# Kernel tuning notes

Hardware: AMD Instinct MI355X
Metric: run time of the kernel (lower is better)

The kernel has to match this reference:

```python
import jax, jax.numpy as jnp
import numpy as np
from jax import lax

B, A, H, W = 16, 9, 128, 128
STRIDE = 16
MIN_SIZE = 16.0


def _generate_anchors():
    base = 16.0
    ratios = np.array([0.5, 1.0, 2.0])
    scales = np.array([8.0, 16.0, 32.0])
    ctr = (base - 1.0) / 2.0
    size = base * base
    ws0 = np.round(np.sqrt(size / ratios))
    hs0 = np.round(ws0 * ratios)
    ws = (ws0[:, None] * scales[None, :]).reshape(-1)  # [9]
    hs = (hs0[:, None] * scales[None, :]).reshape(-1)
    base_anchors = np.stack([ctr - 0.5 * (ws - 1), ctr - 0.5 * (hs - 1),
                             ctr + 0.5 * (ws - 1), ctr + 0.5 * (hs - 1)], axis=1)  # [9,4]
    sx = np.arange(W) * STRIDE
    sy = np.arange(H) * STRIDE
    shift_x, shift_y = np.meshgrid(sx, sy)  # [H,W]
    shifts = np.stack([shift_x, shift_y, shift_x, shift_y], axis=-1).reshape(H * W, 1, 4)
    return (shifts + base_anchors[None]).reshape(-1, 4).astype(np.float32)  # [H*W*A,4]


def setup_inputs() -> dict:
    key = jax.random.key(0)
    k1, k2 = jax.random.split(key)
    scores = jax.random.normal(k1, (B, 2 * A, H, W), jnp.float32)
    bbox_deltas = jax.random.normal(k2, (B, 4 * A, H, W), jnp.float32) * 0.1
    anchors = jnp.asarray(_generate_anchors())
    im_info = jnp.tile(jnp.array([H * STRIDE, W * STRIDE, 1.0, 1.0], jnp.float32), (B, 1))
    return {"scores": scores, "bbox_deltas": bbox_deltas, "anchors": anchors,
            "im_info": im_info, "num_anchors": A, "pre_nms": 2000, "post_nms": 300,
            "nms_thresh": 0.7}


def _iou_matrix(b):
    x1, y1, x2, y2 = b[:, 0], b[:, 1], b[:, 2], b[:, 3]
    area = (x2 - x1 + 1.0) * (y2 - y1 + 1.0)
    iw = jnp.maximum(jnp.minimum(x2[:, None], x2[None, :]) - jnp.maximum(x1[:, None], x1[None, :]) + 1.0, 0.0)
    ih = jnp.maximum(jnp.minimum(y2[:, None], y2[None, :]) - jnp.maximum(y1[:, None], y1[None, :]) + 1.0, 0.0)
    inter = iw * ih
    return inter / (area[:, None] + area[None, :] - inter)


def reference(scores, bbox_deltas, anchors, im_info, num_anchors, pre_nms, post_nms, nms_thresh):
    batch = bbox_deltas.shape[0]
    feat_w = scores.shape[3]
    # deltas -> [B, H*W*A, 4]
    deltas = bbox_deltas.transpose(0, 2, 3, 1).reshape(batch, -1, 4)
    # fg/bg softmax exactly as in the module
    s = jax.nn.softmax(scores.reshape(batch, 2, -1, feat_w), axis=1)
    s = s.reshape(batch, num_anchors * 2, -1, feat_w)[:, num_anchors:, :, :]
    s = s.transpose(0, 2, 3, 1).reshape(batch, -1)  # [B, H*W*A]
    anc = jnp.broadcast_to(anchors.reshape(1, -1, 4), deltas.shape)
    # bbox_transform_inv
    widths = anc[..., 2] - anc[..., 0] + 1.0
    heights = anc[..., 3] - anc[..., 1] + 1.0
    ctr_x = anc[..., 0] + 0.5 * widths
    ctr_y = anc[..., 1] + 0.5 * heights
    dx, dy, dw, dh = deltas[..., 0], deltas[..., 1], deltas[..., 2], deltas[..., 3]
    pcx = dx * widths + ctr_x
    pcy = dy * heights + ctr_y
    pw = jnp.exp(dw) * widths
    ph = jnp.exp(dh) * heights
    proposals = jnp.stack([pcx - 0.5 * pw, pcy - 0.5 * ph, pcx + 0.5 * pw, pcy + 0.5 * ph], axis=-1)
    # clip_boxes to image extent (im_info = [h, w, sy, sx])
    w_max = (im_info[:, 1] - 1.0)[:, None]
    h_max = (im_info[:, 0] - 1.0)[:, None]
    proposals = jnp.stack([
        jnp.clip(proposals[..., 0], 0.0, w_max),
        jnp.clip(proposals[..., 1], 0.0, h_max),
        jnp.clip(proposals[..., 2], 0.0, w_max),
        jnp.clip(proposals[..., 3], 0.0, h_max)], axis=-1)

    ar = jnp.arange(pre_nms)

    def per_image(props, scr, info):
        ws = props[:, 2] - props[:, 0] + 1.0
        hs = props[:, 3] - props[:, 1] + 1.0
        valid = (ws >= MIN_SIZE * info[3]) & (hs >= MIN_SIZE * info[2])
        masked = jnp.where(valid, scr, -jnp.inf)
        vals, idx = lax.top_k(masked, pre_nms)  # sort desc + truncate to pre_nms
        boxes = props[idx]  # [pre_nms, 4], score-sorted
        live = jnp.isfinite(vals)  # drop filtered boxes if fewer than pre_nms survive
        iou = _iou_matrix(boxes)  # [pre_nms, pre_nms]
        def body(i, keep):
            sup = keep[i] & (iou[i] > nms_thresh) & (ar > i)
            return keep & (~sup)
        keep = lax.fori_loop(0, pre_nms, body, live)  # greedy NMS over sorted boxes
        pos = jnp.where(keep, jnp.cumsum(keep) - 1, post_nms)
        kept = jnp.zeros((post_nms, 4), boxes.dtype).at[pos].set(boxes, mode='drop')
        return kept

    kept = jax.vmap(per_image)(proposals, s, im_info)  # [B, post_nms, 4]
    bidx = jnp.broadcast_to(jnp.arange(batch, dtype=kept.dtype)[:, None, None], (batch, post_nms, 1))
    output = jnp.concatenate([bidx, kept], axis=-1)  # [B, post_nms, 5]
    return output, proposals
```

## Files before the change

### kernel.cpp

```cpp
#include <hip/hip_runtime.h>
#include <stdint.h>

#define B_ 16
#define A_ 9
#define H_ 128
#define W_ 128
#define HW_ (H_*W_)
#define N_ (HW_*A_)
#define PRE_ 2000
#define POST_ 300
#define CAND_CAP 4096
#define SEG_ 32

typedef unsigned int u32;
typedef unsigned long long u64;

#define OFF_STATE  0ull
#define OFF_HIST0  1024ull
#define OFF_HIST1  (OFF_HIST0 + 16384ull)
#define OFF_KEYS   (OFF_HIST1 + 16384ull)
#define OFF_CAND   (OFF_KEYS + (u64)B_*N_*4)
#define OFF_SELBOX (OFF_CAND + (u64)B_*CAND_CAP*8)
#define OFF_LIVE   (OFF_SELBOX + (u64)B_*PRE_*16)
#define OFF_SUPP   (OFF_LIVE + (u64)B_*32*8)

__device__ __forceinline__ u32 mono_key(float f) {
    u32 u = __float_as_uint(f);
    return (u & 0x80000000u) ? ~u : (u | 0x80000000u);
}

__device__ __forceinline__ void wave_select256(const u32* __restrict__ hh, u32 need,
                                               u32* __restrict__ out) {
    int lane = threadIdx.x & 63;
    uint4 hv = ((const uint4*)hh)[lane];
    u32 psum = hv.x + hv.y + hv.z + hv.w;
    u32 s = psum;
    #pragma unroll
    for (int off = 1; off < 64; off <<= 1) {
        u32 o = (u32)__shfl_down((int)s, off);
        if (lane + off < 64) s += o;
    }
    u32 S_next = (u32)__shfl_down((int)s, 1);
    if (lane == 63) S_next = 0;
    u32 above[4], cnt[4];
    above[3] = S_next;             cnt[3] = hv.w;
    above[2] = S_next + hv.w;      cnt[2] = hv.z;
    above[1] = above[2] + hv.z;    cnt[1] = hv.y;
    above[0] = above[1] + hv.y;    cnt[0] = hv.x;
    #pragma unroll
    for (int j = 3; j >= 0; --j) {
        if (above[j] < need && above[j] + cnt[j] >= need) {
            out[0] = (u32)(4*lane + j);
            out[1] = need - above[j];
        }
    }
}

__global__ __launch_bounds__(576) void decode_kernel(
        const float* __restrict__ scores,
        const float* __restrict__ deltas,
        const float* __restrict__ anchors,
        const float* __restrict__ im_info,
        float* __restrict__ outprop,
        u32* __restrict__ keys,
        u32* __restrict__ hist0) {
    __shared__ float4 tile[9][65];
    __shared__ float4 sbase[A_];
    __shared__ u32 h[256];
    int tid = threadIdx.x;
    int a = tid >> 6, lane = tid & 63;
    if (tid < A_) sbase[tid] = ((const float4*)anchors)[tid];
    if (tid < 256) h[tid] = 0;
    __syncthreads();

    int b  = blockIdx.x >> 8;
    int pb = blockIdx.x & 255;
    int p0 = pb << 6;
    int p  = p0 + lane;

    float s0 = scores[((b*2*A_ + a)      << 14) + p];
    float s1 = scores[((b*2*A_ + A_ + a) << 14) + p];
    float m  = fmaxf(s0, s1);
    float e0 = expf(s0 - m);
    float e1 = expf(s1 - m);
    float fg = e1 / (e0 + e1);

    float4 base = sbase[a];
    int ix = p & (W_-1), iy = p >> 7;
    float sx = (float)(ix * 16), sy = (float)(iy * 16);
    float ax1 = base.x + sx, ay1 = base.y + sy, ax2 = base.z + sx, ay2 = base.w + sy;

    float w  = ax2 - ax1 + 1.0f;
    float h_ = ay2 - ay1 + 1.0f;
    float cx = ax1 + 0.5f*w;
    float cy = ay1 + 0.5f*h_;

    const float* dbase = deltas + (u64)(((b*4*A_ + 4*a) << 14) + p);
    float dx = dbase[0];
    float dy = dbase[HW_];
    float dw = dbase[2*HW_];
    float dh = dbase[3*HW_];

    float pcx = dx*w  + cx;
    float pcy = dy*h_ + cy;
    float pw  = expf(dw)*w;
    float ph  = expf(dh)*h_;
    float x1 = pcx - 0.5f*pw, y1 = pcy - 0.5f*ph;
    float x2 = pcx + 0.5f*pw, y2 = pcy + 0.5f*ph;

    float wmax = im_info[b*4 + 1] - 1.0f;
    float hmax = im_info[b*4 + 0] - 1.0f;
    x1 = fminf(fmaxf(x1, 0.0f), wmax);
    y1 = fminf(fmaxf(y1, 0.0f), hmax);
    x2 = fminf(fmaxf(x2, 0.0f), wmax);
    y2 = fminf(fmaxf(y2, 0.0f), hmax);

    tile[a][lane] = make_float4(x1, y1, x2, y2);

    float bw = x2 - x1 + 1.0f;
    float bh = y2 - y1 + 1.0f;
    bool valid = (bw >= 16.0f*im_info[b*4 + 3]) && (bh >= 16.0f*im_info[b*4 + 2]);
    float sc = valid ? fg : -__builtin_inff();
    u32 k = mono_key(sc);
    keys[((u64)(b*A_ + a) << 14) + p] = k;
    atomicAdd(&h[k >> 24], 1u);
    __syncthreads();

    int a2 = tid % 9, pl = tid / 9;
    ((float4*)outprop)[(u64)b*N_ + p0*9 + tid] = tile[a2][pl];

    if (tid < 256 && h[tid]) atomicAdd(&hist0[b*256 + tid], h[tid]);
}

__global__ __launch_bounds__(1024) void hist16_kernel(
        const u32* __restrict__ keys, const u32* __restrict__ hist0,
        u32* __restrict__ hist1) {
    int b = blockIdx.x >> 4;
    int slice = blockIdx.x & 15;
    int tid = threadIdx.x;
    __shared__ u32 sel[2];
    __shared__ u32 h[256];
    if (tid < 64) wave_select256(hist0 + b*256, (u32)PRE_, sel);
    for (int i = tid; i < 256; i += 1024) h[i] = 0;
    __syncthreads();
    u32 pfx = sel[0];
    const u32* kb = keys + (u64)b*N_ + slice*(N_/16);
    for (int n = tid; n < N_/16; n += 1024) {
        u32 k = kb[n];
        if ((k >> 24) == pfx) atomicAdd(&h[(k >> 16) & 255u], 1u);
    }
    __syncthreads();
    for (int i = tid; i < 256; i += 1024)
        if (h[i]) atomicAdd(&hist1[b*256 + i], h[i]);
}

__global__ __launch_bounds__(1024) void collect_kernel(
        const u32* __restrict__ keys, const u32* __restrict__ hist0,
        const u32* __restrict__ hist1, u32* __restrict__ state,
        u64* __restrict__ cand) {
    int b = blockIdx.x >> 4;
    int slice = blockIdx.x & 15;
    int tid = threadIdx.x;
    int wave = tid >> 6, lane = tid & 63;
    __shared__ u32 sel8[2], sel16[2];
    __shared__ u32 wbase[16];
    __shared__ u32 s_base;
    if (tid < 64) wave_select256(hist0 + b*256, (u32)PRE_, sel8);
    __syncthreads();
    if (tid < 64) wave_select256(hist1 + b*256, sel8[1], sel16);
    __syncthreads();
    u32 T = (sel8[0] << 24) | (sel16[0] << 16);

    const u32* kb = keys + (u64)b*N_ + slice*(N_/16);
    u64* cb = cand + (u64)b*CAND_CAP;

    u32 kreg[9];
    int c = 0;
    #pragma unroll
    for (int r = 0; r < 9; ++r) {
        kreg[r] = kb[tid + r*1024];
        c += (kreg[r] >= T) ? 1 : 0;
    }

    int x = c;
    #pragma unroll
    for (int off = 1; off < 64; off <<= 1) {
        int y = __shfl_up(x, off);
        if (lane >= off) x += y;
    }
    if (lane == 63) wbase[wave] = (u32)x;
    __syncthreads();
    if (tid == 0) {
        u32 acc = 0;
        #pragma unroll
        for (int w2 = 0; w2 < 16; ++w2) { u32 t2 = wbase[w2]; wbase[w2] = acc; acc += t2; }
        s_base = acc ? atomicAdd(&state[b*8 + 2], acc) : 0u;
    }
    __syncthreads();

    u32 pos = s_base + wbase[wave] + (u32)(x - c);
    #pragma unroll
    for (int r = 0; r < 9; ++r) {
        if (kreg[r] >= T) {
            int idx = slice*(N_/16) + tid + r*1024;
            u32 n = (u32)((idx & (HW_-1))*A_ + (idx >> 14));
            if (pos < CAND_CAP) cb[pos] = ((u64)kreg[r] << 32) | (u32)(~n);
            pos++;
        }
    }
}

__global__ __launch_bounds__(1024) void rank_kernel(
        const u64* __restrict__ cand, const u32* __restrict__ state,
        const float* __restrict__ outprop,
        float4* __restrict__ selbox, u32* __restrict__ selkey) {
    int bi = blockIdx.x;
    int b = bi >> 4, chunk = bi & 15;
    int tid = threadIdx.x;
    int q = tid >> 8, ti = tid & 255;
    __shared__ __align__(16) u64 sc[CAND_CAP];
    __shared__ u32 prank[256];

    u32 cnt = state[b*8 + 2];
    if (cnt > CAND_CAP) cnt = CAND_CAP;
    const u64* cb = cand + (u64)b*CAND_CAP;
    for (int j = tid; j < CAND_CAP; j += 1024) sc[j] = (j < (int)cnt) ? cb[j] : 0ull;
    if (tid < 256) prank[tid] = 0;
    __syncthreads();

    int i = (chunk << 8) + ti;
    u64 mine = sc[i];

    int pairs = ((int)cnt + 1) >> 1;
    int pq = (pairs + 3) >> 2;
    int p0 = q * pq;
    int p1 = p0 + pq; if (p1 > pairs) p1 = pairs;
    const ulonglong2* sl = (const ulonglong2*)sc;
    u32 c = 0;
    #pragma unroll 8
    for (int p = p0; p < p1; ++p) {
        ulonglong2 v = sl[p];
        c += (v.x > mine) ? 1u : 0u;
        c += (v.y > mine) ? 1u : 0u;
    }
    if (c) atomicAdd(&prank[ti], c);
    __syncthreads();

    if (q == 0 && i < (int)cnt) {
        u32 rank = prank[ti];
        if (rank < PRE_) {
            u32 n = ~(u32)mine;
            float4 box = ((const float4*)outprop)[(u64)b*N_ + n];
            selbox[(u64)b*PRE_ + rank] = box;
            selkey[b*2048 + rank] = (u32)(mine >> 32);
        }
    }
}

__global__ __launch_bounds__(256) void iou_kernel(
        const float4* __restrict__ selbox, const float* __restrict__ thrp,
        u64* __restrict__ supp) {
    int bi = blockIdx.x;
    int b = bi / 250;
    int rbase = (bi % 250) * 8;
    int c0 = rbase >> 8;
    int tid = threadIdx.x;
    __shared__ float4 box[PRE_];
    for (int i = (c0 << 8) + tid; i < PRE_; i += 256) box[i] = selbox[(u64)b*PRE_ + i];
    __syncthreads();
    float thresh = thrp[0];
    int wv = tid >> 6, lane = tid & 63;

    float4 p[8]; float ai[8];
    #pragma unroll
    for (int r = 0; r < 8; ++r) {
        p[r]  = box[rbase + r];
        ai[r] = (p[r].z - p[r].x + 1.f) * (p[r].w - p[r].y + 1.f);
    }
    for (int c = c0; c < 8; ++c) {
        int j = c*256 + tid;
        bool inb = (j < PRE_);
        float4 q = box[inb ? j : 0];
        float aj = (q.z - q.x + 1.f) * (q.w - q.y + 1.f);
        #pragma unroll
        for (int r = 0; r < 8; ++r) {
            float iw = fminf(p[r].z, q.z) - fmaxf(p[r].x, q.x) + 1.f;
            float ih = fminf(p[r].w, q.w) - fmaxf(p[r].y, q.y) + 1.f;
            float inter = fmaxf(iw, 0.f) * ih;
            float su = ai[r] + aj;
            float un = su - inter;
            float m  = __fmaf_rn(-thresh, un, inter);
            bool pred = m > 0.0f;
            if (__any(fabsf(m) <= 2.0f)) {
                pred = (inter / un) > thresh;
            }
            pred = pred && inb;
            u64 ball = __ballot(pred);
            if (lane == 0)
                supp[((u64)(b*PRE_ + rbase + r))*32 + (c*4 + wv)] = ball;
        }
    }
}

__global__ __launch_bounds__(256, 1) void scan_kernel(
        const u64* __restrict__ supp, const u32* __restrict__ selkey,
        const float4* __restrict__ selbox, float* __restrict__ out0) {
    int b = blockIdx.x;
    int tid = threadIdx.x;
    int wave = tid >> 6, lane = tid & 63;

    __shared__ u64 rbuf[2][64][33];
    __shared__ u64 lwords[32];
    __shared__ u64 keptmask[SEG_];
    __shared__ int kept[POST_];
    __shared__ int s_kc;

    #pragma unroll
    for (int k = 0; k < 8; ++k) {
        int r = k*256 + tid;
        u32 kk = selkey[b*2048 + r];
        u64 bal = __ballot((r < PRE_) && (kk >= 0x80000000u));
        if (lane == 0) lwords[k*4 + wave] = bal;
    }
    if (tid < SEG_) keptmask[tid] = 0ull;
    if (tid == 0) s_kc = 0;

    const u64* sb = supp + (u64)b*PRE_*32;
    int widx = tid - 64;

    u64 gr[11];
    if (wave != 0) {
        #pragma unroll
        for (int k = 0; k < 11; ++k) {
            int f = k*192 + widx;
            if (f < 2048) gr[k] = sb[(u64)(f >> 5)*32 + (f & 31)];
        }
        #pragma unroll
        for (int k = 0; k < 11; ++k) {
            int f = k*192 + widx;
            if (f < 2048) rbuf[0][f >> 5][f & 31] = gr[k];
        }
        #pragma unroll
        for (int k = 0; k < 11; ++k) {
            int f = k*192 + widx;
            if (f < 2048) gr[k] = sb[(u64)(64 + (f >> 5))*32 + (f & 31)];
        }
    }
    __syncthreads();

    u64 aliveW = 0ull;
    if (wave == 0 && lane < 32) aliveW = lwords[lane];
    int kc = 0;
    int ll = lane & 31;

    for (int g = 0; g < SEG_; ++g) {
        int cur = g & 1;
        if (wave != 0) {
            if (g + 1 < SEG_) {
                #pragma unroll
                for (int k = 0; k < 11; ++k) {
                    int f = k*192 + widx;
                    if (f < 2048) rbuf[cur ^ 1][f >> 5][f & 31] = gr[k];
                }
            }
            if (g + 2 < SEG_) {
                #pragma unroll
                for (int k = 0; k < 11; ++k) {
                    int f = k*192 + widx;
                    if (f < 2048) {
                        int row = ((g + 2) << 6) + (f >> 5);
                        if (row > PRE_ - 1) row = PRE_ - 1;
                        gr[k] = sb[(u64)row*32 + (f & 31)];
                    }
                }
            }
        } else {
            u64 dj = rbuf[cur][lane][g];
            u32 djlo = (u32)dj, djhi = (u32)(dj >> 32);
            u32 alo = __builtin_amdgcn_readlane((u32)aliveW, g);
            u32 ahi = __builtin_amdgcn_readlane((u32)(aliveW >> 32), g);
            u64 a_s = ((u64)ahi << 32) | alo;
            if (a_s) {
                u64 ks = 0ull;
                while (a_s && kc < POST_) {
                    int i = (int)__builtin_ctzll(a_s);
                    u32 kml = __builtin_amdgcn_readlane(djlo, i);
                    u32 kmh = __builtin_amdgcn_readlane(djhi, i);
                    u64 km = ((u64)kmh << 32) | kml;
                    ks |= (1ull << i);
                    kc++;
                    a_s &= ~km;
                    a_s &= ~(1ull << i);
                }
                if (lane == 0) keptmask[g] = ks;
                if (kc < POST_) {
                    u64 t = ks, orr = 0ull;
                    while (t) {
                        int i0 = (int)__builtin_ctzll(t);
                        #define GJ(n) int j##n = t ? (int)__builtin_ctzll(t) : i0; if (t) t &= t - 1;
                        GJ(0) GJ(1) GJ(2) GJ(3) GJ(4) GJ(5) GJ(6) GJ(7)
                        #undef GJ
                        u64 r0 = rbuf[cur][j0][ll];
                        u64 r1 = rbuf[cur][j1][ll];
                        u64 r2 = rbuf[cur][j2][ll];
                        u64 r3 = rbuf[cur][j3][ll];
                        u64 r4 = rbuf[cur][j4][ll];
                        u64 r5 = rbuf[cur][j5][ll];
                        u64 r6 = rbuf[cur][j6][ll];
                        u64 r7 = rbuf[cur][j7][ll];
                        orr |= ((r0 | r1) | (r2 | r3)) | ((r4 | r5) | (r6 | r7));
                    }
                    aliveW &= ~orr;
                }
            }
            if (lane == 0) s_kc = kc;
        }
        __syncthreads();
        bool done = (wave == 0) ? (kc >= POST_) : (s_kc >= POST_);
        if (done) break;
    }

    if (wave == 0) {
        u64 w = (lane < 32) ? keptmask[lane] : 0ull;
        int pc = (int)__builtin_popcountll(w);
        int x = pc;
        #pragma unroll
        for (int off = 1; off < 64; off <<= 1) {
            int y = __shfl_up(x, off);
            if (lane >= off) x += y;
        }
        int pr = x - pc;
        u64 t = w;
        int c = 0;
        while (t) {
            int bit = (int)__builtin_ctzll(t);
            t &= t - 1;
            int pos = pr + c; c++;
            if (pos < POST_) kept[pos] = lane*64 + bit;
        }
    }
    __syncthreads();

    int kc2 = s_kc;
    for (int r = tid; r < POST_; r += 256) {
        int i = (r < kc2) ? kept[r] : -1;
        float o1 = 0.f, o2 = 0.f, o3 = 0.f, o4 = 0.f;
        if (i >= 0) {
            float4 bx = selbox[(u64)b*PRE_ + i];
            o1 = bx.x; o2 = bx.y; o3 = bx.z; o4 = bx.w;
        }
        float* rowp = out0 + (u64)(b*POST_ + r)*5;
        rowp[0] = (float)b;
        rowp[1] = o1; rowp[2] = o2; rowp[3] = o3; rowp[4] = o4;
    }
}

extern "C" void kernel_launch(void* const* d_in, const int* in_sizes, int n_in,
                              void* d_out, int out_size, void* d_ws, size_t ws_size,
                              hipStream_t stream) {
    const float* scores  = (const float*)d_in[0];
    const float* deltas  = (const float*)d_in[1];
    const float* anchors = (const float*)d_in[2];
    const float* im_info = (const float*)d_in[3];
    const float* thrp    = (const float*)d_in[7];

    float* out0    = (float*)d_out;
    float* outprop = out0 + (u64)B_*POST_*5;

    char* ws = (char*)d_ws;
    u32*    state  = (u32*)   (ws + OFF_STATE);
    u32*    hist0  = (u32*)   (ws + OFF_HIST0);
    u32*    hist1  = (u32*)   (ws + OFF_HIST1);
    u32*    keys   = (u32*)   (ws + OFF_KEYS);
    u64*    cand   = (u64*)   (ws + OFF_CAND);
    float4* selbox = (float4*)(ws + OFF_SELBOX);
    u64*    supp   = (u64*)   (ws + OFF_SUPP);
    u32*    selkey = (u32*)   (ws + OFF_KEYS);

    hipMemsetAsync(ws, 0, OFF_KEYS, stream);

    decode_kernel<<<B_*256, 576, 0, stream>>>(scores, deltas, anchors, im_info, outprop, keys, hist0);
    hist16_kernel<<<B_*16, 1024, 0, stream>>>(keys, hist0, hist1);
    collect_kernel<<<B_*16, 1024, 0, stream>>>(keys, hist0, hist1, state, cand);
    rank_kernel<<<B_*16, 1024, 0, stream>>>(cand, state, outprop, selbox, selkey);
    iou_kernel<<<B_*250, 256, 0, stream>>>(selbox, thrp, supp);
    scan_kernel<<<B_, 256, 0, stream>>>(supp, selkey, selbox, out0);
}
```

Baseline: 222.7 us.

## Fuse histogram, collect, rank, IoU and NMS scan into one cooperative kernel

Replaces the five post-decode kernels with a single cooperative kernel launched on 256 blocks of 1024 threads, separating the stages with grid-wide syncs and sharing one shared-memory union across stages. Keys are loaded into registers once and reused for both the second histogram and candidate collection, so the keys array is no longer read twice. The IoU stage is remapped so each block covers several 8-row strips, and the scan stage runs on the first 16 blocks with more loader waves. The aim is to cut per-launch overhead and redundant global reads. In exchange it adds grid-sync cost, requires co-residency of all blocks, and the 1024-thread launch bounds may raise register pressure in the IoU phase.

```diff
diff --git a/kernel.cpp b/kernel.cpp
--- a/kernel.cpp
+++ b/kernel.cpp
@@ -1,5 +1,8 @@
 #include <hip/hip_runtime.h>
+#include <hip/hip_cooperative_groups.h>
 #include <stdint.h>
+
+namespace cg = cooperative_groups;
 
 #define B_ 16
 #define A_ 9
@@ -132,326 +135,306 @@
     if (tid < 256 && h[tid]) atomicAdd(&hist0[b*256 + tid], h[tid]);
 }
 
-__global__ __launch_bounds__(1024) void hist16_kernel(
+__global__ __launch_bounds__(1024, 4) void fused_kernel(
         const u32* __restrict__ keys, const u32* __restrict__ hist0,
-        u32* __restrict__ hist1) {
-    int b = blockIdx.x >> 4;
-    int slice = blockIdx.x & 15;
-    int tid = threadIdx.x;
-    __shared__ u32 sel[2];
-    __shared__ u32 h[256];
-    if (tid < 64) wave_select256(hist0 + b*256, (u32)PRE_, sel);
-    for (int i = tid; i < 256; i += 1024) h[i] = 0;
-    __syncthreads();
-    u32 pfx = sel[0];
-    const u32* kb = keys + (u64)b*N_ + slice*(N_/16);
-    for (int n = tid; n < N_/16; n += 1024) {
-        u32 k = kb[n];
-        if ((k >> 24) == pfx) atomicAdd(&h[(k >> 16) & 255u], 1u);
-    }
-    __syncthreads();
-    for (int i = tid; i < 256; i += 1024)
-        if (h[i]) atomicAdd(&hist1[b*256 + i], h[i]);
-}
-
-__global__ __launch_bounds__(1024) void collect_kernel(
-        const u32* __restrict__ keys, const u32* __restrict__ hist0,
-        const u32* __restrict__ hist1, u32* __restrict__ state,
-        u64* __restrict__ cand) {
-    int b = blockIdx.x >> 4;
-    int slice = blockIdx.x & 15;
+        u32* __restrict__ hist1, u32* __restrict__ state,
+        u64* __restrict__ cand, const float* __restrict__ outprop,
+        float4* __restrict__ selbox, u32* __restrict__ selkey,
+        const float* __restrict__ thrp, u64* __restrict__ supp,
+        float* __restrict__ out0) {
+    cg::grid_group grid = cg::this_grid();
+    int bi = blockIdx.x;
+    int b = bi >> 4, slice = bi & 15;
     int tid = threadIdx.x;
     int wave = tid >> 6, lane = tid & 63;
-    __shared__ u32 sel8[2], sel16[2];
-    __shared__ u32 wbase[16];
-    __shared__ u32 s_base;
-    if (tid < 64) wave_select256(hist0 + b*256, (u32)PRE_, sel8);
+
+    __shared__ union SM {
+        struct { u32 h[256]; } p1;
+        struct { u64 sc[CAND_CAP]; u32 prank[256]; } p3;
+        struct { float4 box[PRE_]; } p4;
+        struct { u64 rbuf[2][64][33]; u64 lwords[32];
+                 u64 keptmask[SEG_]; int kept[POST_]; int s_kc; } p5;
+    } sm;
+    __shared__ u32 xsel8[2], xsel16[2], xwbase[16];
+    __shared__ u32 xsbase;
+
+    if (tid < 64) wave_select256(hist0 + b*256, (u32)PRE_, xsel8);
+    for (int i = tid; i < 256; i += 1024) sm.p1.h[i] = 0;
     __syncthreads();
-    if (tid < 64) wave_select256(hist1 + b*256, sel8[1], sel16);
-    __syncthreads();
-    u32 T = (sel8[0] << 24) | (sel16[0] << 16);
-
+    u32 pfx = xsel8[0];
     const u32* kb = keys + (u64)b*N_ + slice*(N_/16);
-    u64* cb = cand + (u64)b*CAND_CAP;
-
     u32 kreg[9];
-    int c = 0;
     #pragma unroll
     for (int r = 0; r < 9; ++r) {
         kreg[r] = kb[tid + r*1024];
-        c += (kreg[r] >= T) ? 1 : 0;
-    }
-
-    int x = c;
-    #pragma unroll
-    for (int off = 1; off < 64; off <<= 1) {
-        int y = __shfl_up(x, off);
-        if (lane >= off) x += y;
-    }
-    if (lane == 63) wbase[wave] = (u32)x;
+        if ((kreg[r] >> 24) == pfx) atomicAdd(&sm.p1.h[(kreg[r] >> 16) & 255u], 1u);
+    }
     __syncthreads();
-    if (tid == 0) {
-        u32 acc = 0;
+    for (int i = tid; i < 256; i += 1024)
+        if (sm.p1.h[i]) atomicAdd(&hist1[b*256 + i], sm.p1.h[i]);
+
+    grid.sync();
+
+    if (tid < 64) wave_select256(hist1 + b*256, xsel8[1], xsel16);
+    __syncthreads();
+    {
+        u32 T = (xsel8[0] << 24) | (xsel16[0] << 16);
+        int c = 0;
         #pragma unroll
-        for (int w2 = 0; w2 < 16; ++w2) { u32 t2 = wbase[w2]; wbase[w2] = acc; acc += t2; }
-        s_base = acc ? atomicAdd(&state[b*8 + 2], acc) : 0u;
-    }
-    __syncthreads();
-
-    u32 pos = s_base + wbase[wave] + (u32)(x - c);
-    #pragma unroll
-    for (int r = 0; r < 9; ++r) {
-        if (kreg[r] >= T) {
-            int idx = slice*(N_/16) + tid + r*1024;
-            u32 n = (u32)((idx & (HW_-1))*A_ + (idx >> 14));
-            if (pos < CAND_CAP) cb[pos] = ((u64)kreg[r] << 32) | (u32)(~n);
-            pos++;
-        }
-    }
-}
-
-__global__ __launch_bounds__(1024) void rank_kernel(
-        const u64* __restrict__ cand, const u32* __restrict__ state,
-        const float* __restrict__ outprop,
-        float4* __restrict__ selbox, u32* __restrict__ selkey) {
-    int bi = blockIdx.x;
-    int b = bi >> 4, chunk = bi & 15;
-    int tid = threadIdx.x;
-    int q = tid >> 8, ti = tid & 255;
-    __shared__ __align__(16) u64 sc[CAND_CAP];
-    __shared__ u32 prank[256];
-
-    u32 cnt = state[b*8 + 2];
-    if (cnt > CAND_CAP) cnt = CAND_CAP;
-    const u64* cb = cand + (u64)b*CAND_CAP;
-    for (int j = tid; j < CAND_CAP; j += 1024) sc[j] = (j < (int)cnt) ? cb[j] : 0ull;
-    if (tid < 256) prank[tid] = 0;
-    __syncthreads();
-
-    int i = (chunk << 8) + ti;
-    u64 mine = sc[i];
-
-    int pairs = ((int)cnt + 1) >> 1;
-    int pq = (pairs + 3) >> 2;
-    int p0 = q * pq;
-    int p1 = p0 + pq; if (p1 > pairs) p1 = pairs;
-    const ulonglong2* sl = (const ulonglong2*)sc;
-    u32 c = 0;
-    #pragma unroll 8
-    for (int p = p0; p < p1; ++p) {
-        ulonglong2 v = sl[p];
-        c += (v.x > mine) ? 1u : 0u;
-        c += (v.y > mine) ? 1u : 0u;
-    }
-    if (c) atomicAdd(&prank[ti], c);
-    __syncthreads();
-
-    if (q == 0 && i < (int)cnt) {
-        u32 rank = prank[ti];
-        if (rank < PRE_) {
-            u32 n = ~(u32)mine;
-            float4 box = ((const float4*)outprop)[(u64)b*N_ + n];
-            selbox[(u64)b*PRE_ + rank] = box;
-            selkey[b*2048 + rank] = (u32)(mine >> 32);
-        }
-    }
-}
-
-__global__ __launch_bounds__(256) void iou_kernel(
-        const float4* __restrict__ selbox, const float* __restrict__ thrp,
-        u64* __restrict__ supp) {
-    int bi = blockIdx.x;
-    int b = bi / 250;
-    int rbase = (bi % 250) * 8;
-    int c0 = rbase >> 8;
-    int tid = threadIdx.x;
-    __shared__ float4 box[PRE_];
-    for (int i = (c0 << 8) + tid; i < PRE_; i += 256) box[i] = selbox[(u64)b*PRE_ + i];
-    __syncthreads();
-    float thresh = thrp[0];
-    int wv = tid >> 6, lane = tid & 63;
-
-    float4 p[8]; float ai[8];
-    #pragma unroll
-    for (int r = 0; r < 8; ++r) {
-        p[r]  = box[rbase + r];
-        ai[r] = (p[r].z - p[r].x + 1.f) * (p[r].w - p[r].y + 1.f);
-    }
-    for (int c = c0; c < 8; ++c) {
-        int j = c*256 + tid;
-        bool inb = (j < PRE_);
-        float4 q = box[inb ? j : 0];
-        float aj = (q.z - q.x + 1.f) * (q.w - q.y + 1.f);
-        #pragma unroll
-        for (int r = 0; r < 8; ++r) {
-            float iw = fminf(p[r].z, q.z) - fmaxf(p[r].x, q.x) + 1.f;
-            float ih = fminf(p[r].w, q.w) - fmaxf(p[r].y, q.y) + 1.f;
-            float inter = fmaxf(iw, 0.f) * ih;
-            float su = ai[r] + aj;
-            float un = su - inter;
-            float m  = __fmaf_rn(-thresh, un, inter);
-            bool pred = m > 0.0f;
-            if (__any(fabsf(m) <= 2.0f)) {
-                pred = (inter / un) > thresh;
-            }
-            pred = pred && inb;
-            u64 ball = __ballot(pred);
-            if (lane == 0)
-                supp[((u64)(b*PRE_ + rbase + r))*32 + (c*4 + wv)] = ball;
-        }
-    }
-}
-
-__global__ __launch_bounds__(256, 1) void scan_kernel(
-        const u64* __restrict__ supp, const u32* __restrict__ selkey,
-        const float4* __restrict__ selbox, float* __restrict__ out0) {
-    int b = blockIdx.x;
-    int tid = threadIdx.x;
-    int wave = tid >> 6, lane = tid & 63;
-
-    __shared__ u64 rbuf[2][64][33];
-    __shared__ u64 lwords[32];
-    __shared__ u64 keptmask[SEG_];
-    __shared__ int kept[POST_];
-    __shared__ int s_kc;
-
-    #pragma unroll
-    for (int k = 0; k < 8; ++k) {
-        int r = k*256 + tid;
-        u32 kk = selkey[b*2048 + r];
-        u64 bal = __ballot((r < PRE_) && (kk >= 0x80000000u));
-        if (lane == 0) lwords[k*4 + wave] = bal;
-    }
-    if (tid < SEG_) keptmask[tid] = 0ull;
-    if (tid == 0) s_kc = 0;
-
-    const u64* sb = supp + (u64)b*PRE_*32;
-    int widx = tid - 64;
-
-    u64 gr[11];
-    if (wave != 0) {
-        #pragma unroll
-        for (int k = 0; k < 11; ++k) {
-            int f = k*192 + widx;
-            if (f < 2048) gr[k] = sb[(u64)(f >> 5)*32 + (f & 31)];
-        }
-        #pragma unroll
-        for (int k = 0; k < 11; ++k) {
-            int f = k*192 + widx;
-            if (f < 2048) rbuf[0][f >> 5][f & 31] = gr[k];
-        }
-        #pragma unroll
-        for (int k = 0; k < 11; ++k) {
-            int f = k*192 + widx;
-            if (f < 2048) gr[k] = sb[(u64)(64 + (f >> 5))*32 + (f & 31)];
-        }
-    }
-    __syncthreads();
-
-    u64 aliveW = 0ull;
-    if (wave == 0 && lane < 32) aliveW = lwords[lane];
-    int kc = 0;
-    int ll = lane & 31;
-
-    for (int g = 0; g < SEG_; ++g) {
-        int cur = g & 1;
-        if (wave != 0) {
-            if (g + 1 < SEG_) {
-                #pragma unroll
-                for (int k = 0; k < 11; ++k) {
-                    int f = k*192 + widx;
-                    if (f < 2048) rbuf[cur ^ 1][f >> 5][f & 31] = gr[k];
-                }
-            }
-            if (g + 2 < SEG_) {
-                #pragma unroll
-                for (int k = 0; k < 11; ++k) {
-                    int f = k*192 + widx;
-                    if (f < 2048) {
-                        int row = ((g + 2) << 6) + (f >> 5);
-                        if (row > PRE_ - 1) row = PRE_ - 1;
-                        gr[k] = sb[(u64)row*32 + (f & 31)];
-                    }
-                }
-            }
-        } else {
-            u64 dj = rbuf[cur][lane][g];
-            u32 djlo = (u32)dj, djhi = (u32)(dj >> 32);
-            u32 alo = __builtin_amdgcn_readlane((u32)aliveW, g);
-            u32 ahi = __builtin_amdgcn_readlane((u32)(aliveW >> 32), g);
-            u64 a_s = ((u64)ahi << 32) | alo;
-            if (a_s) {
-                u64 ks = 0ull;
-                while (a_s && kc < POST_) {
-                    int i = (int)__builtin_ctzll(a_s);
-                    u32 kml = __builtin_amdgcn_readlane(djlo, i);
-                    u32 kmh = __builtin_amdgcn_readlane(djhi, i);
-                    u64 km = ((u64)kmh << 32) | kml;
-                    ks |= (1ull << i);
-                    kc++;
-                    a_s &= ~km;
-                    a_s &= ~(1ull << i);
-                }
-                if (lane == 0) keptmask[g] = ks;
-                if (kc < POST_) {
-                    u64 t = ks, orr = 0ull;
-                    while (t) {
-                        int i0 = (int)__builtin_ctzll(t);
-                        #define GJ(n) int j##n = t ? (int)__builtin_ctzll(t) : i0; if (t) t &= t - 1;
-                        GJ(0) GJ(1) GJ(2) GJ(3) GJ(4) GJ(5) GJ(6) GJ(7)
-                        #undef GJ
-                        u64 r0 = rbuf[cur][j0][ll];
-                        u64 r1 = rbuf[cur][j1][ll];
-                        u64 r2 = rbuf[cur][j2][ll];
-                        u64 r3 = rbuf[cur][j3][ll];
-                        u64 r4 = rbuf[cur][j4][ll];
-                        u64 r5 = rbuf[cur][j5][ll];
-                        u64 r6 = rbuf[cur][j6][ll];
-                        u64 r7 = rbuf[cur][j7][ll];
-                        orr |= ((r0 | r1) | (r2 | r3)) | ((r4 | r5) | (r6 | r7));
-                    }
-                    aliveW &= ~orr;
-                }
-            }
-            if (lane == 0) s_kc = kc;
-        }
-        __syncthreads();
-        bool done = (wave == 0) ? (kc >= POST_) : (s_kc >= POST_);
-        if (done) break;
-    }
-
-    if (wave == 0) {
-        u64 w = (lane < 32) ? keptmask[lane] : 0ull;
-        int pc = (int)__builtin_popcountll(w);
-        int x = pc;
+        for (int r = 0; r < 9; ++r) c += (kreg[r] >= T) ? 1 : 0;
+        int x = c;
         #pragma unroll
         for (int off = 1; off < 64; off <<= 1) {
             int y = __shfl_up(x, off);
             if (lane >= off) x += y;
         }
-        int pr = x - pc;
-        u64 t = w;
-        int c = 0;
-        while (t) {
-            int bit = (int)__builtin_ctzll(t);
-            t &= t - 1;
-            int pos = pr + c; c++;
-            if (pos < POST_) kept[pos] = lane*64 + bit;
-        }
-    }
-    __syncthreads();
-
-    int kc2 = s_kc;
-    for (int r = tid; r < POST_; r += 256) {
-        int i = (r < kc2) ? kept[r] : -1;
-        float o1 = 0.f, o2 = 0.f, o3 = 0.f, o4 = 0.f;
-        if (i >= 0) {
-            float4 bx = selbox[(u64)b*PRE_ + i];
-            o1 = bx.x; o2 = bx.y; o3 = bx.z; o4 = bx.w;
-        }
-        float* rowp = out0 + (u64)(b*POST_ + r)*5;
-        rowp[0] = (float)b;
-        rowp[1] = o1; rowp[2] = o2; rowp[3] = o3; rowp[4] = o4;
+        if (lane == 63) xwbase[wave] = (u32)x;
+        __syncthreads();
+        if (tid == 0) {
+            u32 acc = 0;
+            #pragma unroll
+            for (int w2 = 0; w2 < 16; ++w2) { u32 t2 = xwbase[w2]; xwbase[w2] = acc; acc += t2; }
+            xsbase = acc ? atomicAdd(&state[b*8 + 2], acc) : 0u;
+        }
+        __syncthreads();
+        u32 pos = xsbase + xwbase[wave] + (u32)(x - c);
+        u64* cb = cand + (u64)b*CAND_CAP;
+        #pragma unroll
+        for (int r = 0; r < 9; ++r) {
+            if (kreg[r] >= T) {
+                int idx = slice*(N_/16) + tid + r*1024;
+                u32 n = (u32)((idx & (HW_-1))*A_ + (idx >> 14));
+                if (pos < CAND_CAP) cb[pos] = ((u64)kreg[r] << 32) | (u32)(~n);
+                pos++;
+            }
+        }
+    }
+
+    grid.sync();
+
+    {
+        int q = tid >> 8, ti = tid & 255;
+        u32 cnt = state[b*8 + 2];
+        if (cnt > CAND_CAP) cnt = CAND_CAP;
+        const u64* cb = cand + (u64)b*CAND_CAP;
+        for (int j = tid; j < CAND_CAP; j += 1024) sm.p3.sc[j] = (j < (int)cnt) ? cb[j] : 0ull;
+        if (tid < 256) sm.p3.prank[tid] = 0;
+        __syncthreads();
+        int i = (slice << 8) + ti;
+        u64 mine = sm.p3.sc[i];
+        int pairs = ((int)cnt + 1) >> 1;
+        int pq = (pairs + 3) >> 2;
+        int p0 = q * pq;
+        int p1 = p0 + pq; if (p1 > pairs) p1 = pairs;
+        const ulonglong2* sl = (const ulonglong2*)sm.p3.sc;
+        u32 c = 0;
+        #pragma unroll 8
+        for (int p = p0; p < p1; ++p) {
+            ulonglong2 v = sl[p];
+            c += (v.x > mine) ? 1u : 0u;
+            c += (v.y > mine) ? 1u : 0u;
+        }
+        if (c) atomicAdd(&sm.p3.prank[ti], c);
+        __syncthreads();
+        if (q == 0 && i < (int)cnt) {
+            u32 rank = sm.p3.prank[ti];
+            if (rank < PRE_) {
+                u32 n = ~(u32)mine;
+                float4 box = ((const float4*)outprop)[(u64)b*N_ + n];
+                selbox[(u64)b*PRE_ + rank] = box;
+                selkey[b*2048 + rank] = (u32)(mine >> 32);
+            }
+        }
+    }
+
+    grid.sync();
+
+    {
+        float thresh = thrp[0];
+        for (int i = tid; i < PRE_; i += 1024) sm.p4.box[i] = selbox[(u64)b*PRE_ + i];
+        __syncthreads();
+        int q = tid >> 8, tq = tid & 255;
+        int wv = (tq >> 6), ln = tq & 63;
+        for (int it = 0; it < 4; ++it) {
+            int strip = slice*4 + q + it*64;
+            if (strip >= 250) break;
+            int rbase = strip * 8;
+            int c0 = rbase >> 8;
+            float4 p[8]; float ai[8];
+            #pragma unroll
+            for (int r = 0; r < 8; ++r) {
+                p[r]  = sm.p4.box[rbase + r];
+                ai[r] = (p[r].z - p[r].x + 1.f) * (p[r].w - p[r].y + 1.f);
+            }
+            for (int c = c0; c < 8; ++c) {
+                int j = c*256 + tq;
+                bool inb = (j < PRE_);
+                float4 qq = sm.p4.box[inb ? j : 0];
+                float aj = (qq.z - qq.x + 1.f) * (qq.w - qq.y + 1.f);
+                #pragma unroll
+                for (int r = 0; r < 8; ++r) {
+                    float iw = fminf(p[r].z, qq.z) - fmaxf(p[r].x, qq.x) + 1.f;
+                    float ih = fminf(p[r].w, qq.w) - fmaxf(p[r].y, qq.y) + 1.f;
+                    float inter = fmaxf(iw, 0.f) * ih;
+                    float su = ai[r] + aj;
+                    float un = su - inter;
+                    float mm = __fmaf_rn(-thresh, un, inter);
+                    bool pred = mm > 0.0f;
+                    if (__any(fabsf(mm) <= 2.0f)) {
+                        pred = (inter / un) > thresh;
+                    }
+                    pred = pred && inb;
+                    u64 ball = __ballot(pred);
+                    if (ln == 0)
+                        supp[((u64)(b*PRE_ + rbase + r))*32 + (c*4 + wv)] = ball;
+                }
+            }
+        }
+    }
+
+    grid.sync();
+
+    if (bi >= B_) return;
+    int b5 = bi;
+    {
+        #pragma unroll
+        for (int k = 0; k < 2; ++k) {
+            int r = k*1024 + tid;
+            u32 kk = selkey[b5*2048 + r];
+            u64 bal = __ballot((r < PRE_) && (kk >= 0x80000000u));
+            if (lane == 0) sm.p5.lwords[k*16 + wave] = bal;
+        }
+        if (tid < SEG_) sm.p5.keptmask[tid] = 0ull;
+        if (tid == 0) sm.p5.s_kc = 0;
+
+        const u64* sb = supp + (u64)b5*PRE_*32;
+        int widx = tid - 64;
+
+        u64 gr[3];
+        if (wave != 0) {
+            #pragma unroll
+            for (int k = 0; k < 3; ++k) {
+                int f = k*960 + widx;
+                if (f < 2048) gr[k] = sb[(u64)(f >> 5)*32 + (f & 31)];
+            }
+            #pragma unroll
+            for (int k = 0; k < 3; ++k) {
+                int f = k*960 + widx;
+                if (f < 2048) sm.p5.rbuf[0][f >> 5][f & 31] = gr[k];
+            }
+            #pragma unroll
+            for (int k = 0; k < 3; ++k) {
+                int f = k*960 + widx;
+                if (f < 2048) gr[k] = sb[(u64)(64 + (f >> 5))*32 + (f & 31)];
+            }
+        }
+        __syncthreads();
+
+        u64 aliveW = 0ull;
+        if (wave == 0 && lane < 32) aliveW = sm.p5.lwords[lane];
+        int kc = 0;
+        int ll = lane & 31;
+
+        for (int g = 0; g < SEG_; ++g) {
+            int cur = g & 1;
+            if (wave != 0) {
+                if (g + 1 < SEG_) {
+                    #pragma unroll
+                    for (int k = 0; k < 3; ++k) {
+                        int f = k*960 + widx;
+                        if (f < 2048) sm.p5.rbuf[cur ^ 1][f >> 5][f & 31] = gr[k];
+                    }
+                }
+                if (g + 2 < SEG_) {
+                    #pragma unroll
+                    for (int k = 0; k < 3; ++k) {
+                        int f = k*960 + widx;
+                        if (f < 2048) {
+                            int row = ((g + 2) << 6) + (f >> 5);
+                            if (row > PRE_ - 1) row = PRE_ - 1;
+                            gr[k] = sb[(u64)row*32 + (f & 31)];
+                        }
+                    }
+                }
+            } else {
+                u64 dj = sm.p5.rbuf[cur][lane][g];
+                u32 djlo = (u32)dj, djhi = (u32)(dj >> 32);
+                u32 alo = __builtin_amdgcn_readlane((u32)aliveW, g);
+                u32 ahi = __builtin_amdgcn_readlane((u32)(aliveW >> 32), g);
+                u64 a_s = ((u64)ahi << 32) | alo;
+                if (a_s) {
+                    u64 ks = 0ull;
+                    while (a_s && kc < POST_) {
+                        int i = (int)__builtin_ctzll(a_s);
+                        u32 kml = __builtin_amdgcn_readlane(djlo, i);
+                        u32 kmh = __builtin_amdgcn_readlane(djhi, i);
+                        u64 km = ((u64)kmh << 32) | kml;
+                        ks |= (1ull << i);
+                        kc++;
+                        a_s &= ~km;
+                        a_s &= ~(1ull << i);
+                    }
+                    if (lane == 0) sm.p5.keptmask[g] = ks;
+                    if (kc < POST_) {
+                        u64 t = ks, orr = 0ull;
+                        while (t) {
+                            int i0 = (int)__builtin_ctzll(t);
+                            #define GJ(n) int j##n = t ? (int)__builtin_ctzll(t) : i0; if (t) t &= t - 1;
+                            GJ(0) GJ(1) GJ(2) GJ(3) GJ(4) GJ(5) GJ(6) GJ(7)
+                            #undef GJ
+                            u64 r0 = sm.p5.rbuf[cur][j0][ll];
+                            u64 r1 = sm.p5.rbuf[cur][j1][ll];
+                            u64 r2 = sm.p5.rbuf[cur][j2][ll];
+                            u64 r3 = sm.p5.rbuf[cur][j3][ll];
+                            u64 r4 = sm.p5.rbuf[cur][j4][ll];
+                            u64 r5 = sm.p5.rbuf[cur][j5][ll];
+                            u64 r6 = sm.p5.rbuf[cur][j6][ll];
+                            u64 r7 = sm.p5.rbuf[cur][j7][ll];
+                            orr |= ((r0 | r1) | (r2 | r3)) | ((r4 | r5) | (r6 | r7));
+                        }
+                        aliveW &= ~orr;
+                    }
+                }
+                if (lane == 0) sm.p5.s_kc = kc;
+            }
+            __syncthreads();
+            bool done = (wave == 0) ? (kc >= POST_) : (sm.p5.s_kc >= POST_);
+            if (done) break;
+        }
+
+        if (wave == 0) {
+            u64 w = (lane < 32) ? sm.p5.keptmask[lane] : 0ull;
+            int pc = (int)__builtin_popcountll(w);
+            int x = pc;
+            #pragma unroll
+            for (int off = 1; off < 64; off <<= 1) {
+                int y = __shfl_up(x, off);
+                if (lane >= off) x += y;
+            }
+            int pr = x - pc;
+            u64 t = w;
+            int c = 0;
+            while (t) {
+                int bit = (int)__builtin_ctzll(t);
+                t &= t - 1;
+                int pos = pr + c; c++;
+                if (pos < POST_) sm.p5.kept[pos] = lane*64 + bit;
+            }
+        }
+        __syncthreads();
+
+        int kc2 = sm.p5.s_kc;
+        for (int r = tid; r < POST_; r += 1024) {
+            int i = (r < kc2) ? sm.p5.kept[r] : -1;
+            float o1 = 0.f, o2 = 0.f, o3 = 0.f, o4 = 0.f;
+            if (i >= 0) {
+                float4 bx = selbox[(u64)b5*PRE_ + i];
+                o1 = bx.x; o2 = bx.y; o3 = bx.z; o4 = bx.w;
+            }
+            float* rowp = out0 + (u64)(b5*POST_ + r)*5;
+            rowp[0] = (float)b5;
+            rowp[1] = o1; rowp[2] = o2; rowp[3] = o3; rowp[4] = o4;
+        }
     }
 }
 
@@ -480,9 +463,15 @@
     hipMemsetAsync(ws, 0, OFF_KEYS, stream);
 
     decode_kernel<<<B_*256, 576, 0, stream>>>(scores, deltas, anchors, im_info, outprop, keys, hist0);
-    hist16_kernel<<<B_*16, 1024, 0, stream>>>(keys, hist0, hist1);
-    collect_kernel<<<B_*16, 1024, 0, stream>>>(keys, hist0, hist1, state, cand);
-    rank_kernel<<<B_*16, 1024, 0, stream>>>(cand, state, outprop, selbox, selkey);
-    iou_kernel<<<B_*250, 256, 0, stream>>>(selbox, thrp, supp);
-    scan_kernel<<<B_, 256, 0, stream>>>(supp, selkey, selbox, out0);
+
+    const float* outprop_c = outprop;
+    const u32*   keys_c    = keys;
+    const u32*   hist0_c   = hist0;
+    void* kargs[] = {
+        (void*)&keys_c, (void*)&hist0_c, (void*)&hist1, (void*)&state,
+        (void*)&cand, (void*)&outprop_c, (void*)&selbox, (void*)&selkey,
+        (void*)&thrp, (void*)&supp, (void*)&out0
+    };
+    hipLaunchCooperativeKernel((const void*)fused_kernel, dim3(B_*16), dim3(1024),
+                               kargs, 0, stream);
 }
```

After: 345.1 us. 54.9% more time.
